# Optimization experiments

Measured on AMD Instinct MI355X. Metric: run time of the kernel, lower is better.

Reference implementation:

```python
import jax, jax.numpy as jnp
import numpy as np

BATCH, SEQ, D_MODEL, D_STATE = 8, 4096, 128, 128


def setup_inputs() -> dict:
    key = jax.random.key(0)
    ks = jax.random.split(key, 6)
    x = jax.random.normal(ks[0], (BATCH, SEQ, D_MODEL), jnp.float32)
    # Stable (negative) eigenvalues so A_discrete = exp(dt*Lambda) < 1 and powers don't overflow.
    Lam = -(jax.random.uniform(ks[1], (D_STATE,), jnp.float32) * 2.0 + 0.1)
    B = jax.random.normal(ks[2], (D_STATE, D_MODEL), jnp.float32) / np.sqrt(D_STATE)
    C = jax.random.normal(ks[3], (D_MODEL, D_STATE), jnp.float32) / np.sqrt(D_STATE)
    Dv = jax.random.normal(ks[4], (D_MODEL,), jnp.float32)
    log_dt = (jax.random.uniform(ks[5], (D_MODEL,), jnp.float32)
              * (np.log(0.001) - np.log(0.1)) + np.log(0.1)).astype(jnp.float32)
    return {"x": x, "Lam": Lam, "B": B, "C": C, "Dv": Dv, "log_dt": log_dt}


def _s4_forward(x, Lam, B, C, Dv, log_dt):
    # x: (batch, L, M) with transposed=False
    _, L, M = x.shape
    dt = jnp.exp(log_dt)                                    # (M,)
    rate = dt[:, None] * Lam[None, :]                       # (M, N) = log(A_discrete)
    ell = jnp.arange(L, dtype=x.dtype)                      # (L,)
    # powers[m, s, l] = A_discrete[m, s] ** l  (closed form of the sequential cumprod)
    powers = jnp.exp(rate[:, :, None] * ell[None, None, :])  # (M, N, L)
    # Original: einsum('ds,msl->dsl', B, powers) sums over m, giving B[d,s]*Psum[s,l];
    # then einsum('md,dsl->ml', C, .) contracts d and s -> kernel = C @ B @ Psum.
    Psum = powers.sum(axis=0)                               # (N, L)
    kernel = C @ (B @ Psum)                                 # (M, L)
    xt = jnp.transpose(x, (0, 2, 1))                        # (B, M, L)
    n = 2 * L  # zero-padded linear convolution via FFT
    y_fft = jnp.fft.rfft(xt, n=n) * jnp.fft.rfft(kernel, n=n)[None]
    y = jnp.fft.irfft(y_fft, n=n)[..., :L]                  # (B, M, L)
    y = y + Dv[None, :, None] * xt                          # skip connection D*u
    return jnp.transpose(y, (0, 2, 1))                      # (B, L, M)


def reference(x, Lam, B, C, Dv, log_dt):
    return _s4_forward(x, Lam, B, C, Dv, log_dt)
```

## Files before the change

### kernel.cpp

```cpp
#include <hip/hip_runtime.h>
#include <math.h>

#define BATCH 8
#define SEQ   4096
#define DM    128
#define DS    128
#define N2    4096
#define NT    256
#define NTP   256

__device__ __forceinline__ float2 cmulf(float2 a, float2 b) {
    return make_float2(a.x * b.x - a.y * b.y, a.x * b.y + a.y * b.x);
}
__device__ __forceinline__ float2 caddf(float2 a, float2 b) { return make_float2(a.x + b.x, a.y + b.y); }
__device__ __forceinline__ float2 csubf(float2 a, float2 b) { return make_float2(a.x - b.x, a.y - b.y); }
__device__ __forceinline__ float2 conjf2(float2 a) { return make_float2(a.x, -a.y); }
__device__ __forceinline__ float2 cisf(float t) { float s, c; __sincosf(t, &s, &c); return make_float2(c, s); }

__device__ __forceinline__ int nibrev(int k) { return ((k & 15) << 8) | (k & 0xF0) | (k >> 8); }
__device__ __forceinline__ int physi(int a) { return a ^ ((a >> 4) & 15); }
__device__ __forceinline__ int pqslot(int p) { return ((p & 15) << 8) | (p >> 4); }

__device__ __forceinline__ void dft16_fwd(const float2 x[16], float2 Xh[16]) {
    const float2 W[10] = { {1.f,0.f},
        {0.92387953f,-0.38268343f},{0.70710678f,-0.70710678f},{0.38268343f,-0.92387953f},
        {0.f,-1.f},{-0.38268343f,-0.92387953f},{-0.70710678f,-0.70710678f},
        {-0.92387953f,-0.38268343f},{-1.f,0.f},{-0.92387953f,0.38268343f} };
    float2 y[16];
#pragma unroll
    for (int j = 0; j < 4; ++j) {
        float2 a0 = x[j], a1 = x[j+4], a2 = x[j+8], a3 = x[j+12];
        float2 t0 = caddf(a0,a2), t1 = csubf(a0,a2);
        float2 t2 = caddf(a1,a3), t3 = csubf(a1,a3);
        float2 b1 = make_float2(t1.x + t3.y, t1.y - t3.x);
        float2 b3 = make_float2(t1.x - t3.y, t1.y + t3.x);
        y[j]    = caddf(t0,t2);
        y[j+4]  = cmulf(b1, W[j]);
        y[j+8]  = cmulf(csubf(t0,t2), W[2*j]);
        y[j+12] = cmulf(b3, W[3*j]);
    }
#pragma unroll
    for (int g = 0; g < 4; ++g) {
        float2 a0 = y[4*g], a1 = y[4*g+1], a2 = y[4*g+2], a3 = y[4*g+3];
        float2 t0 = caddf(a0,a2), t1 = csubf(a0,a2);
        float2 t2 = caddf(a1,a3), t3 = csubf(a1,a3);
        Xh[4*g]   = caddf(t0,t2);
        Xh[4*g+1] = make_float2(t1.x + t3.y, t1.y - t3.x);
        Xh[4*g+2] = csubf(t0,t2);
        Xh[4*g+3] = make_float2(t1.x - t3.y, t1.y + t3.x);
    }
}
__device__ __forceinline__ void dft16_inv(const float2 x[16], float2 Xh[16]) {
    const float2 W[10] = { {1.f,0.f},
        {0.92387953f,0.38268343f},{0.70710678f,0.70710678f},{0.38268343f,0.92387953f},
        {0.f,1.f},{-0.38268343f,0.92387953f},{-0.70710678f,0.70710678f},
        {-0.92387953f,0.38268343f},{-1.f,0.f},{-0.92387953f,-0.38268343f} };
    float2 y[16];
#pragma unroll
    for (int j = 0; j < 4; ++j) {
        float2 a0 = x[j], a1 = x[j+4], a2 = x[j+8], a3 = x[j+12];
        float2 t0 = caddf(a0,a2), t1 = csubf(a0,a2);
        float2 t2 = caddf(a1,a3), t3 = csubf(a1,a3);
        float2 b1 = make_float2(t1.x - t3.y, t1.y + t3.x);
        float2 b3 = make_float2(t1.x + t3.y, t1.y - t3.x);
        y[j]    = caddf(t0,t2);
        y[j+4]  = cmulf(b1, W[j]);
        y[j+8]  = cmulf(csubf(t0,t2), W[2*j]);
        y[j+12] = cmulf(b3, W[3*j]);
    }
#pragma unroll
    for (int g = 0; g < 4; ++g) {
        float2 a0 = y[4*g], a1 = y[4*g+1], a2 = y[4*g+2], a3 = y[4*g+3];
        float2 t0 = caddf(a0,a2), t1 = csubf(a0,a2);
        float2 t2 = caddf(a1,a3), t3 = csubf(a1,a3);
        Xh[4*g]   = caddf(t0,t2);
        Xh[4*g+1] = make_float2(t1.x - t3.y, t1.y + t3.x);
        Xh[4*g+2] = csubf(t0,t2);
        Xh[4*g+3] = make_float2(t1.x + t3.y, t1.y - t3.x);
    }
}


template<int Q>
__device__ __forceinline__ void stage_fwd(float2* z, int t) {
    float2 x[16], Xh[16];
    int adr[16];
    if (Q == 16) {
        int j = t & 15, top = t >> 4;
#pragma unroll
        for (int r = 0; r < 16; ++r) adr[r] = (top << 8) + (r << 4) + (j ^ r);
    } else {
        int j4 = t & 15;
#pragma unroll
        for (int r = 0; r < 16; ++r) adr[r] = (t << 4) + (j4 ^ r);
    }
#pragma unroll
    for (int r = 0; r < 16; ++r) x[r] = z[adr[r]];
    dft16_fwd(x, Xh);
    if (Q > 1) {
        int j = t & (Q - 1);
        float2 w1 = cisf(-(float)M_PI / (8.0f * (float)Q) * (float)j);
        float2 w = make_float2(1.f, 0.f);
#pragma unroll
        for (int k = 0; k < 16; ++k) {
            int sk = ((k & 3) << 2) | (k >> 2);
            z[adr[k]] = cmulf(Xh[sk], w);
            w = cmulf(w, w1);
        }
    } else {
#pragma unroll
        for (int k = 0; k < 16; ++k) {
            int sk = ((k & 3) << 2) | (k >> 2);
            z[adr[k]] = Xh[sk];
        }
    }
}

template<int Q>
__device__ __forceinline__ void stage_inv(float2* z, int t) {
    float2 x[16], Xh[16];
    int adr[16];
    if (Q == 16) {
        int j = t & 15, top = t >> 4;
#pragma unroll
        for (int r = 0; r < 16; ++r) adr[r] = (top << 8) + (r << 4) + (j ^ r);
    } else {
        int j4 = t & 15;
#pragma unroll
        for (int r = 0; r < 16; ++r) adr[r] = (t << 4) + (j4 ^ r);
    }
    if (Q > 1) {
        int j = t & (Q - 1);
        float2 w1 = cisf((float)M_PI / (8.0f * (float)Q) * (float)j);
        float2 w = make_float2(1.f, 0.f);
#pragma unroll
        for (int k = 0; k < 16; ++k) {
            x[k] = cmulf(z[adr[k]], w);
            w = cmulf(w, w1);
        }
    } else {
#pragma unroll
        for (int k = 0; k < 16; ++k) x[k] = z[adr[k]];
    }
    dft16_inv(x, Xh);
#pragma unroll
    for (int r = 0; r < 16; ++r) {
        int sr = ((r & 3) << 2) | (r >> 2);
        z[adr[r]] = Xh[sr];
    }
}

__device__ __forceinline__ void fwd_first(float2* z, const float2* __restrict__ vrow, int t) {
    float2 x[16], Xh[16];
#pragma unroll
    for (int r = 0; r < 8; ++r) x[r] = vrow[t + (r << 8)];
#pragma unroll
    for (int r = 8; r < 16; ++r) x[r] = make_float2(0.f, 0.f);
    dft16_fwd(x, Xh);
    int b0 = t ^ ((t >> 4) & 15);
    float2 w1 = cisf(-(float)M_PI / 2048.0f * (float)t);
    float2 w = make_float2(1.f, 0.f);
#pragma unroll
    for (int k = 0; k < 16; ++k) {
        int sk = ((k & 3) << 2) | (k >> 2);
        z[b0 + (k << 8)] = cmulf(Xh[sk], w);
        w = cmulf(w, w1);
    }
}

__device__ __forceinline__ void inv_last_store(const float2* z, float2* __restrict__ xrow,
                                               int t, float dv) {
    float2 x[16], Xh[16];
    int b0 = t ^ ((t >> 4) & 15);
    float2 w1 = cisf((float)M_PI / 2048.0f * (float)t);
    float2 w = make_float2(1.f, 0.f);
#pragma unroll
    for (int k = 0; k < 16; ++k) {
        x[k] = cmulf(z[b0 + (k << 8)], w);
        w = cmulf(w, w1);
    }
    dft16_inv(x, Xh);
    const float invN = 1.0f / 4096.0f;
#pragma unroll
    for (int r = 0; r < 8; ++r) {
        int sr = ((r & 3) << 2) | (r >> 2);
        float2 res = Xh[sr];
        float2 xv = xrow[t + (r << 8)];
        xrow[t + (r << 8)] = make_float2(res.x * invN + dv * xv.x, res.y * invN + dv * xv.y);
    }
}

__device__ __forceinline__ void pq_one(float2 Kk, float2 Kkp, float thk,
                                       float2 fap, float2 fbp,
                                       float2* P, float2* Q) {
    float2 e  = cisf(-thk);
    float2 fa = make_float2(0.5f * (1.f + e.y), -0.5f * e.x);
    float2 fb = make_float2(0.5f * (1.f - e.y),  0.5f * e.x);
    float2 ak = cmulf(Kk, fa), bk = cmulf(Kk, fb);
    float2 apv = cmulf(Kkp, fap), bpv = cmulf(Kkp, fbp);
    float2 g = make_float2(0.5f * (1.f + e.y), 0.5f * e.x);
    float2 h = make_float2(0.5f * (1.f - e.y), -0.5f * e.x);
    *P = caddf(cmulf(g, ak), cmulf(h, conjf2(bpv)));
    *Q = caddf(cmulf(g, bk), cmulf(h, conjf2(apv)));
}
__device__ __forceinline__ void pq_pair(float2 Kk, float2 Kkp, float thk, float thkp,
                                        float2* Pk, float2* Qk, float2* Pkp, float2* Qkp) {
    float2 e  = cisf(-thk);
    float2 ep = cisf(-thkp);
    float2 fa  = make_float2(0.5f * (1.f + e.y),  -0.5f * e.x);
    float2 fb  = make_float2(0.5f * (1.f - e.y),   0.5f * e.x);
    float2 fap = make_float2(0.5f * (1.f + ep.y), -0.5f * ep.x);
    float2 fbp = make_float2(0.5f * (1.f - ep.y),  0.5f * ep.x);
    pq_one(Kk,  Kkp, thk,  fap, fbp, Pk,  Qk);
    pq_one(Kkp, Kk,  thkp, fa,  fb,  Pkp, Qkp);
}

__global__ void __launch_bounds__(NTP) prep_GP(
    const float* __restrict__ Lam, const float* __restrict__ logdt, float* __restrict__ Psum,
    const float* __restrict__ Cm, const float* __restrict__ Bm, float* __restrict__ GT) {
    int bid = blockIdx.x, t = threadIdx.x;
    if (bid < 256) {
        __shared__ float E[DM];
        int s = bid >> 1, half = bid & 1;
        if (t < DM) E[t] = __expf(logdt[t]) * Lam[s];
        __syncthreads();
        int l0 = t + 2048 * half;
        float acc[8] = {0.f,0.f,0.f,0.f,0.f,0.f,0.f,0.f};
        for (int m = 0; m < DM; ++m) {
            float e = E[m];
            float w = __expf(e * (float)l0);
            float r = __expf(e * 256.0f);
#pragma unroll
            for (int i = 0; i < 8; ++i) { acc[i] += w; w *= r; }
        }
#pragma unroll
        for (int i = 0; i < 8; ++i) Psum[s * SEQ + l0 + 256 * i] = acc[i];
    } else {
        int gid = (bid - 256) * NTP + t;
        int m = gid >> 7, j = gid & 127;
        float acc = 0.f;
        for (int i = 0; i < DS; ++i) acc += Cm[m * DS + i] * Bm[i * DM + j];
        GT[j * DM + m] = acc;
    }
}

__global__ void prep_K2(const float* __restrict__ GT, const float* __restrict__ Psum,
                        float* __restrict__ K) {
    __shared__ float4 PT[DS][4];
    int l0 = blockIdx.x * 16;
    int t = threadIdx.x;
    for (int idx = t; idx < 512; idx += NTP) {
        int s = idx >> 2, q = idx & 3;
        PT[s][q] = ((const float4*)(Psum + s * SEQ + l0))[q];
    }
    __syncthreads();
    int m = t & 127, half = t >> 7;
    float acc[8] = {0.f,0.f,0.f,0.f,0.f,0.f,0.f,0.f};
    for (int s = 0; s < DS; ++s) {
        float g = GT[s * DM + m];
        float4 p0 = PT[s][half * 2], p1 = PT[s][half * 2 + 1];
        acc[0] += g * p0.x; acc[1] += g * p0.y; acc[2] += g * p0.z; acc[3] += g * p0.w;
        acc[4] += g * p1.x; acc[5] += g * p1.y; acc[6] += g * p1.z; acc[7] += g * p1.w;
    }
    float4* kp = (float4*)(K + (size_t)m * SEQ + l0 + half * 8);
    kp[0] = make_float4(acc[0], acc[1], acc[2], acc[3]);
    kp[1] = make_float4(acc[4], acc[5], acc[6], acc[7]);
}

__global__ void __launch_bounds__(NT, 4) fftK_PQ(const float* __restrict__ K,
                                                 float4* __restrict__ PQ) {
    __shared__ __align__(16) float2 z[N2];
    int t = threadIdx.x, m = blockIdx.x;
    const float2* krow = (const float2*)(K + (size_t)m * SEQ);

    fwd_first(z, krow, t);  __syncthreads();
    stage_fwd<16>(z, t);    __syncthreads();
    stage_fwd<1>(z, t);     __syncthreads();

    float4* dst = PQ + (size_t)m * 4096;
#pragma unroll
    for (int c = 0; c < 8; ++c) {
        int pos = (t << 4) | c;
        float2 Pk, Qk, Pkp, Qkp;
        if (pos == 0) {
            float2 v0 = z[0];
            float2 v2 = z[8];
            float2 Ku0    = make_float2(v0.x + v0.y, 0.f);
            float2 Ku4096 = make_float2(v0.x - v0.y, 0.f);
            float2 Ku2048 = conjf2(v2);
            float2 Pd, Qd;
            pq_pair(Ku0, Ku4096, 0.f, (float)M_PI, &Pk, &Qk, &Pd, &Qd);
            float th2 = 0.5f * (float)M_PI;
            pq_pair(Ku2048, Ku2048, th2, th2, &Pkp, &Qkp, &Pd, &Qd);
            dst[pqslot(0)] = make_float4(Pk.x, Pk.y, Qk.x, Qk.y);
            dst[pqslot(8)] = make_float4(Pkp.x, Pkp.y, Qkp.x, Qkp.y);
        } else {
            int k  = nibrev(pos);
            int kp = 4096 - k;
            int ppos = nibrev(kp);
            float2 va = z[physi(pos)];
            float2 vb = z[physi(ppos)];
            float thk  = (float)M_PI * (float)k / 4096.0f;
            float thkp = (float)M_PI - thk;
            float2 e  = cisf(-thk);
            float2 cb = conjf2(vb);
            float2 s  = caddf(va, cb), d = csubf(va, cb);
            float2 pr = cmulf(e, d);
            float2 Kuk = make_float2(0.5f * (s.x + pr.y), 0.5f * (s.y - pr.x));
            float2 ep = make_float2(-e.x, e.y);
            float2 ca = conjf2(va);
            float2 s2 = caddf(vb, ca), d2 = csubf(vb, ca);
            float2 p2 = cmulf(ep, d2);
            float2 Kukp = make_float2(0.5f * (s2.x + p2.y), 0.5f * (s2.y - p2.x));
            pq_pair(Kuk, Kukp, thk, thkp, &Pk, &Qk, &Pkp, &Qkp);
            dst[pqslot(pos)]  = make_float4(Pk.x, Pk.y, Qk.x, Qk.y);
            dst[pqslot(ppos)] = make_float4(Pkp.x, Pkp.y, Qkp.x, Qkp.y);
        }
    }
}

__global__ void __launch_bounds__(NT, 4) conv16(float* __restrict__ xt,
                                                const float4* __restrict__ PQ,
                                                const float* __restrict__ Dv) {
    __shared__ __align__(16) float2 z[N2];
    int t = threadIdx.x;
    int m = blockIdx.x & (DM - 1);
    int b = blockIdx.x >> 7;
    float2* xrow = (float2*)(xt + (((size_t)b * DM + m) << 12));

    fwd_first(z, xrow, t);  __syncthreads();
    stage_fwd<16>(z, t);    __syncthreads();
    stage_fwd<1>(z, t);     __syncthreads();

    float2 x[16];
    {
        const float4* pq = PQ + (size_t)m * 4096;
        int j4 = t & 15;
#pragma unroll
        for (int r = 0; r < 16; ++r) {
            int pos = (t << 4) | r;
            float2 va = z[(t << 4) + (r ^ j4)];
            int k  = nibrev(pos);
            int kp = (4096 - k) & 4095;
            float2 vb = z[physi(nibrev(kp))];
            float4 co = pq[(r << 8) | t];
            x[r] = caddf(cmulf(make_float2(co.x, co.y), va),
                         cmulf(make_float2(co.z, co.w), conjf2(vb)));
        }
    }
    __syncthreads();
    {
        float2 Xh[16];
        dft16_inv(x, Xh);
        int j4 = t & 15;
#pragma unroll
        for (int r = 0; r < 16; ++r) {
            int sr = ((r & 3) << 2) | (r >> 2);
            z[(t << 4) + (r ^ j4)] = Xh[sr];
        }
    }
    __syncthreads();

    stage_inv<16>(z, t);    __syncthreads();
    inv_last_store(z, xrow, t, Dv[m]);
}

__global__ void transpose_xin(const float* __restrict__ x, float* __restrict__ xt) {
    __shared__ float tile[32][33];
    int b = blockIdx.z;
    int l0 = blockIdx.x * 32, m0 = blockIdx.y * 32;
    int t = threadIdx.x;
    int lr = t >> 3, mc4 = (t & 7) * 4;
    float4 v = *(const float4*)&x[(size_t)b * SEQ * DM + (size_t)(l0 + lr) * DM + m0 + mc4];
    tile[lr][mc4 + 0] = v.x; tile[lr][mc4 + 1] = v.y;
    tile[lr][mc4 + 2] = v.z; tile[lr][mc4 + 3] = v.w;
    __syncthreads();
    int mr = t >> 3, lc4 = (t & 7) * 4;
    float4 o = make_float4(tile[lc4 + 0][mr], tile[lc4 + 1][mr],
                           tile[lc4 + 2][mr], tile[lc4 + 3][mr]);
    *(float4*)&xt[(size_t)b * DM * SEQ + (size_t)(m0 + mr) * SEQ + l0 + lc4] = o;
}

__global__ void transpose_yout(const float* __restrict__ yt, float* __restrict__ out) {
    __shared__ float tile[32][33];
    int b = blockIdx.z;
    int l0 = blockIdx.x * 32, m0 = blockIdx.y * 32;
    int t = threadIdx.x;
    int mr = t >> 3, lc4 = (t & 7) * 4;
    float4 v = *(const float4*)&yt[(size_t)b * DM * SEQ + (size_t)(m0 + mr) * SEQ + l0 + lc4];
    tile[mr][lc4 + 0] = v.x; tile[mr][lc4 + 1] = v.y;
    tile[mr][lc4 + 2] = v.z; tile[mr][lc4 + 3] = v.w;
    __syncthreads();
    int lr = t >> 3, mc4 = (t & 7) * 4;
    float4 o = make_float4(tile[mc4 + 0][lr], tile[mc4 + 1][lr],
                           tile[mc4 + 2][lr], tile[mc4 + 3][lr]);
    *(float4*)&out[(size_t)b * SEQ * DM + (size_t)(l0 + lr) * DM + m0 + mc4] = o;
}

extern "C" void kernel_launch(void* const* d_in, const int* in_sizes, int n_in,
                              void* d_out, int out_size, void* d_ws, size_t ws_size,
                              hipStream_t stream) {
    const float* x     = (const float*)d_in[0];
    const float* Lam   = (const float*)d_in[1];
    const float* Bm    = (const float*)d_in[2];
    const float* Cm    = (const float*)d_in[3];
    const float* Dv    = (const float*)d_in[4];
    const float* logdt = (const float*)d_in[5];
    float* out = (float*)d_out;

    float*  ws   = (float*)d_ws;
    float*  xt   = ws;
    float4* PQ   = (float4*)(ws + 4194304);
    float*  K    = ws + 4194304 + 2097152;
    float*  Psum = K + 524288;
    float*  GT   = Psum + 524288;

    hipLaunchKernelGGL(prep_GP,        dim3(320),        dim3(NTP),  0, stream,
                       Lam, logdt, Psum, Cm, Bm, GT);
    hipLaunchKernelGGL(prep_K2,        dim3(256),        dim3(NTP),  0, stream, GT, Psum, K);
    hipLaunchKernelGGL(fftK_PQ,        dim3(128),        dim3(NT),   0, stream, K, PQ);
    hipLaunchKernelGGL(transpose_xin,  dim3(128, 4, 8),  dim3(NT),   0, stream, x, xt);
    hipLaunchKernelGGL(conv16,         dim3(1024),       dim3(NT),   0, stream, xt, PQ, Dv);
    hipLaunchKernelGGL(transpose_yout, dim3(128, 4, 8),  dim3(NT),   0, stream, xt, out);
}
```

Before: 129.8 us.

## Fuse input transpose into prep kernel and prune FFT butterflies

Merges the input transpose into the prep kernel launch, which removes one kernel launch. It specializes the radix-16 stages: the forward first stage skips the zero-padded half and the inverse last stage computes only the eight outputs that are kept. The first-stage output stays in registers so it is not reloaded from shared memory, and twiddles come from two half-length recurrences. fftK_PQ is split across twice as many blocks, each handling half of the PQ epilogue; the forward FFT of K is now computed redundantly in both blocks.

```diff
diff --git a/kernel.cpp b/kernel.cpp
--- a/kernel.cpp
+++ b/kernel.cpp
@@ -21,6 +21,31 @@
 __device__ __forceinline__ int physi(int a) { return a ^ ((a >> 4) & 15); }
 __device__ __forceinline__ int pqslot(int p) { return ((p & 15) << 8) | (p >> 4); }
 
+__device__ __forceinline__ void dft16_fwd_l2(const float2 y[16], float2 Xh[16]) {
+#pragma unroll
+    for (int g = 0; g < 4; ++g) {
+        float2 a0 = y[4*g], a1 = y[4*g+1], a2 = y[4*g+2], a3 = y[4*g+3];
+        float2 t0 = caddf(a0,a2), t1 = csubf(a0,a2);
+        float2 t2 = caddf(a1,a3), t3 = csubf(a1,a3);
+        Xh[4*g]   = caddf(t0,t2);
+        Xh[4*g+1] = make_float2(t1.x + t3.y, t1.y - t3.x);
+        Xh[4*g+2] = csubf(t0,t2);
+        Xh[4*g+3] = make_float2(t1.x - t3.y, t1.y + t3.x);
+    }
+}
+__device__ __forceinline__ void dft16_inv_l2(const float2 y[16], float2 Xh[16]) {
+#pragma unroll
+    for (int g = 0; g < 4; ++g) {
+        float2 a0 = y[4*g], a1 = y[4*g+1], a2 = y[4*g+2], a3 = y[4*g+3];
+        float2 t0 = caddf(a0,a2), t1 = csubf(a0,a2);
+        float2 t2 = caddf(a1,a3), t3 = csubf(a1,a3);
+        Xh[4*g]   = caddf(t0,t2);
+        Xh[4*g+1] = make_float2(t1.x - t3.y, t1.y + t3.x);
+        Xh[4*g+2] = csubf(t0,t2);
+        Xh[4*g+3] = make_float2(t1.x + t3.y, t1.y - t3.x);
+    }
+}
+
 __device__ __forceinline__ void dft16_fwd(const float2 x[16], float2 Xh[16]) {
     const float2 W[10] = { {1.f,0.f},
         {0.92387953f,-0.38268343f},{0.70710678f,-0.70710678f},{0.38268343f,-0.92387953f},
@@ -39,17 +64,28 @@
         y[j+8]  = cmulf(csubf(t0,t2), W[2*j]);
         y[j+12] = cmulf(b3, W[3*j]);
     }
-#pragma unroll
-    for (int g = 0; g < 4; ++g) {
-        float2 a0 = y[4*g], a1 = y[4*g+1], a2 = y[4*g+2], a3 = y[4*g+3];
-        float2 t0 = caddf(a0,a2), t1 = csubf(a0,a2);
-        float2 t2 = caddf(a1,a3), t3 = csubf(a1,a3);
-        Xh[4*g]   = caddf(t0,t2);
-        Xh[4*g+1] = make_float2(t1.x + t3.y, t1.y - t3.x);
-        Xh[4*g+2] = csubf(t0,t2);
-        Xh[4*g+3] = make_float2(t1.x - t3.y, t1.y + t3.x);
-    }
-}
+    dft16_fwd_l2(y, Xh);
+}
+
+__device__ __forceinline__ void dft16_fwd_zh(const float2 x[8], float2 Xh[16]) {
+    const float2 W[10] = { {1.f,0.f},
+        {0.92387953f,-0.38268343f},{0.70710678f,-0.70710678f},{0.38268343f,-0.92387953f},
+        {0.f,-1.f},{-0.38268343f,-0.92387953f},{-0.70710678f,-0.70710678f},
+        {-0.92387953f,-0.38268343f},{-1.f,0.f},{-0.92387953f,0.38268343f} };
+    float2 y[16];
+#pragma unroll
+    for (int j = 0; j < 4; ++j) {
+        float2 a0 = x[j], a1 = x[j+4];
+        float2 b1 = make_float2(a0.x + a1.y, a0.y - a1.x);
+        float2 b3 = make_float2(a0.x - a1.y, a0.y + a1.x);
+        y[j]    = caddf(a0, a1);
+        y[j+4]  = cmulf(b1, W[j]);
+        y[j+8]  = cmulf(csubf(a0, a1), W[2*j]);
+        y[j+12] = cmulf(b3, W[3*j]);
+    }
+    dft16_fwd_l2(y, Xh);
+}
+
 __device__ __forceinline__ void dft16_inv(const float2 x[16], float2 Xh[16]) {
     const float2 W[10] = { {1.f,0.f},
         {0.92387953f,0.38268343f},{0.70710678f,0.70710678f},{0.38268343f,0.92387953f},
@@ -68,79 +104,76 @@
         y[j+8]  = cmulf(csubf(t0,t2), W[2*j]);
         y[j+12] = cmulf(b3, W[3*j]);
     }
+    dft16_inv_l2(y, Xh);
+}
+
+__device__ __forceinline__ void dft16_inv_lo8(const float2 x[16], float2 out8[8]) {
+    const float2 W[10] = { {1.f,0.f},
+        {0.92387953f,0.38268343f},{0.70710678f,0.70710678f},{0.38268343f,0.92387953f},
+        {0.f,1.f},{-0.38268343f,0.92387953f},{-0.70710678f,0.70710678f},
+        {-0.92387953f,0.38268343f},{-1.f,0.f},{-0.92387953f,-0.38268343f} };
+    float2 y[16];
+#pragma unroll
+    for (int j = 0; j < 4; ++j) {
+        float2 a0 = x[j], a1 = x[j+4], a2 = x[j+8], a3 = x[j+12];
+        float2 t0 = caddf(a0,a2), t1 = csubf(a0,a2);
+        float2 t2 = caddf(a1,a3), t3 = csubf(a1,a3);
+        float2 b1 = make_float2(t1.x - t3.y, t1.y + t3.x);
+        float2 b3 = make_float2(t1.x + t3.y, t1.y - t3.x);
+        y[j]    = caddf(t0,t2);
+        y[j+4]  = cmulf(b1, W[j]);
+        y[j+8]  = cmulf(csubf(t0,t2), W[2*j]);
+        y[j+12] = cmulf(b3, W[3*j]);
+    }
 #pragma unroll
     for (int g = 0; g < 4; ++g) {
         float2 a0 = y[4*g], a1 = y[4*g+1], a2 = y[4*g+2], a3 = y[4*g+3];
         float2 t0 = caddf(a0,a2), t1 = csubf(a0,a2);
         float2 t2 = caddf(a1,a3), t3 = csubf(a1,a3);
-        Xh[4*g]   = caddf(t0,t2);
-        Xh[4*g+1] = make_float2(t1.x - t3.y, t1.y + t3.x);
-        Xh[4*g+2] = csubf(t0,t2);
-        Xh[4*g+3] = make_float2(t1.x + t3.y, t1.y - t3.x);
-    }
-}
-
-
-template<int Q>
-__device__ __forceinline__ void stage_fwd(float2* z, int t) {
+        out8[g]   = caddf(t0,t2);
+        out8[4+g] = make_float2(t1.x - t3.y, t1.y + t3.x);
+    }
+}
+
+__device__ __forceinline__ void stage16_fwd(float2* z, int t) {
     float2 x[16], Xh[16];
     int adr[16];
-    if (Q == 16) {
-        int j = t & 15, top = t >> 4;
-#pragma unroll
-        for (int r = 0; r < 16; ++r) adr[r] = (top << 8) + (r << 4) + (j ^ r);
-    } else {
-        int j4 = t & 15;
-#pragma unroll
-        for (int r = 0; r < 16; ++r) adr[r] = (t << 4) + (j4 ^ r);
-    }
+    int j = t & 15, top = t >> 4;
+#pragma unroll
+    for (int r = 0; r < 16; ++r) adr[r] = (top << 8) + (r << 4) + (j ^ r);
 #pragma unroll
     for (int r = 0; r < 16; ++r) x[r] = z[adr[r]];
     dft16_fwd(x, Xh);
-    if (Q > 1) {
-        int j = t & (Q - 1);
-        float2 w1 = cisf(-(float)M_PI / (8.0f * (float)Q) * (float)j);
-        float2 w = make_float2(1.f, 0.f);
-#pragma unroll
-        for (int k = 0; k < 16; ++k) {
-            int sk = ((k & 3) << 2) | (k >> 2);
-            z[adr[k]] = cmulf(Xh[sk], w);
-            w = cmulf(w, w1);
-        }
-    } else {
-#pragma unroll
-        for (int k = 0; k < 16; ++k) {
-            int sk = ((k & 3) << 2) | (k >> 2);
-            z[adr[k]] = Xh[sk];
-        }
-    }
-}
-
-template<int Q>
-__device__ __forceinline__ void stage_inv(float2* z, int t) {
+    float ang = -(float)M_PI / 128.0f * (float)j;
+    float2 w1 = cisf(ang);
+    float2 wa = make_float2(1.f, 0.f);
+    float2 wb = cisf(ang * 8.0f);
+#pragma unroll
+    for (int k = 0; k < 8; ++k) {
+        int sk = ((k & 3) << 2) | (k >> 2);
+        z[adr[k]]     = cmulf(Xh[sk],     wa);
+        z[adr[k + 8]] = cmulf(Xh[sk + 2], wb);
+        wa = cmulf(wa, w1);
+        wb = cmulf(wb, w1);
+    }
+}
+
+__device__ __forceinline__ void stage16_inv(float2* z, int t) {
     float2 x[16], Xh[16];
     int adr[16];
-    if (Q == 16) {
-        int j = t & 15, top = t >> 4;
-#pragma unroll
-        for (int r = 0; r < 16; ++r) adr[r] = (top << 8) + (r << 4) + (j ^ r);
-    } else {
-        int j4 = t & 15;
-#pragma unroll
-        for (int r = 0; r < 16; ++r) adr[r] = (t << 4) + (j4 ^ r);
-    }
-    if (Q > 1) {
-        int j = t & (Q - 1);
-        float2 w1 = cisf((float)M_PI / (8.0f * (float)Q) * (float)j);
-        float2 w = make_float2(1.f, 0.f);
-#pragma unroll
-        for (int k = 0; k < 16; ++k) {
-            x[k] = cmulf(z[adr[k]], w);
-            w = cmulf(w, w1);
-        }
-    } else {
-#pragma unroll
-        for (int k = 0; k < 16; ++k) x[k] = z[adr[k]];
+    int j = t & 15, top = t >> 4;
+#pragma unroll
+    for (int r = 0; r < 16; ++r) adr[r] = (top << 8) + (r << 4) + (j ^ r);
+    float ang = (float)M_PI / 128.0f * (float)j;
+    float2 w1 = cisf(ang);
+    float2 wa = make_float2(1.f, 0.f);
+    float2 wb = cisf(ang * 8.0f);
+#pragma unroll
+    for (int k = 0; k < 8; ++k) {
+        x[k]     = cmulf(z[adr[k]],     wa);
+        x[k + 8] = cmulf(z[adr[k + 8]], wb);
+        wa = cmulf(wa, w1);
+        wb = cmulf(wb, w1);
     }
     dft16_inv(x, Xh);
 #pragma unroll
@@ -150,50 +183,71 @@
     }
 }
 
-__device__ __forceinline__ void fwd_first(float2* z, const float2* __restrict__ vrow, int t) {
+__device__ __forceinline__ void stage1_fwd_keep(float2* z, int t, float2 v[16]) {
     float2 x[16], Xh[16];
-#pragma unroll
-    for (int r = 0; r < 8; ++r) x[r] = vrow[t + (r << 8)];
-#pragma unroll
-    for (int r = 8; r < 16; ++r) x[r] = make_float2(0.f, 0.f);
+    int adr[16];
+    int j4 = t & 15;
+#pragma unroll
+    for (int r = 0; r < 16; ++r) adr[r] = (t << 4) + (j4 ^ r);
+#pragma unroll
+    for (int r = 0; r < 16; ++r) x[r] = z[adr[r]];
     dft16_fwd(x, Xh);
-    int b0 = t ^ ((t >> 4) & 15);
-    float2 w1 = cisf(-(float)M_PI / 2048.0f * (float)t);
-    float2 w = make_float2(1.f, 0.f);
 #pragma unroll
     for (int k = 0; k < 16; ++k) {
         int sk = ((k & 3) << 2) | (k >> 2);
-        z[b0 + (k << 8)] = cmulf(Xh[sk], w);
-        w = cmulf(w, w1);
+        v[k] = Xh[sk];
+        z[adr[k]] = v[k];
+    }
+}
+
+__device__ __forceinline__ void fwd_first(float2* z, const float2* __restrict__ vrow, int t) {
+    float2 x8[8], Xh[16];
+#pragma unroll
+    for (int r = 0; r < 8; ++r) x8[r] = vrow[t + (r << 8)];
+    dft16_fwd_zh(x8, Xh);
+    int b0 = t ^ ((t >> 4) & 15);
+    float ang = -(float)M_PI / 2048.0f * (float)t;
+    float2 w1 = cisf(ang);
+    float2 wa = make_float2(1.f, 0.f);
+    float2 wb = cisf(ang * 8.0f);
+#pragma unroll
+    for (int k = 0; k < 8; ++k) {
+        int sk = ((k & 3) << 2) | (k >> 2);
+        z[b0 + (k << 8)]       = cmulf(Xh[sk],     wa);
+        z[b0 + ((k + 8) << 8)] = cmulf(Xh[sk + 2], wb);
+        wa = cmulf(wa, w1);
+        wb = cmulf(wb, w1);
     }
 }
 
 __device__ __forceinline__ void inv_last_store(const float2* z, float2* __restrict__ xrow,
                                                int t, float dv) {
-    float2 x[16], Xh[16];
+    float2 x[16], out8[8];
     int b0 = t ^ ((t >> 4) & 15);
-    float2 w1 = cisf((float)M_PI / 2048.0f * (float)t);
-    float2 w = make_float2(1.f, 0.f);
-#pragma unroll
-    for (int k = 0; k < 16; ++k) {
-        x[k] = cmulf(z[b0 + (k << 8)], w);
-        w = cmulf(w, w1);
-    }
-    dft16_inv(x, Xh);
+    float ang = (float)M_PI / 2048.0f * (float)t;
+    float2 w1 = cisf(ang);
+    float2 wa = make_float2(1.f, 0.f);
+    float2 wb = cisf(ang * 8.0f);
+#pragma unroll
+    for (int k = 0; k < 8; ++k) {
+        x[k]     = cmulf(z[b0 + (k << 8)],       wa);
+        x[k + 8] = cmulf(z[b0 + ((k + 8) << 8)], wb);
+        wa = cmulf(wa, w1);
+        wb = cmulf(wb, w1);
+    }
+    dft16_inv_lo8(x, out8);
     const float invN = 1.0f / 4096.0f;
 #pragma unroll
     for (int r = 0; r < 8; ++r) {
-        int sr = ((r & 3) << 2) | (r >> 2);
-        float2 res = Xh[sr];
+        float2 res = out8[r];
         float2 xv = xrow[t + (r << 8)];
         xrow[t + (r << 8)] = make_float2(res.x * invN + dv * xv.x, res.y * invN + dv * xv.y);
     }
 }
 
-__device__ __forceinline__ void pq_one(float2 Kk, float2 Kkp, float thk,
-                                       float2 fap, float2 fbp,
-                                       float2* P, float2* Q) {
-    float2 e  = cisf(-thk);
+__device__ __forceinline__ void pq_one_e(float2 Kk, float2 Kkp, float2 e,
+                                         float2 fap, float2 fbp,
+                                         float2* P, float2* Q) {
     float2 fa = make_float2(0.5f * (1.f + e.y), -0.5f * e.x);
     float2 fb = make_float2(0.5f * (1.f - e.y),  0.5f * e.x);
     float2 ak = cmulf(Kk, fa), bk = cmulf(Kk, fb);
@@ -203,24 +257,25 @@
     *P = caddf(cmulf(g, ak), cmulf(h, conjf2(bpv)));
     *Q = caddf(cmulf(g, bk), cmulf(h, conjf2(apv)));
 }
-__device__ __forceinline__ void pq_pair(float2 Kk, float2 Kkp, float thk, float thkp,
-                                        float2* Pk, float2* Qk, float2* Pkp, float2* Qkp) {
-    float2 e  = cisf(-thk);
-    float2 ep = cisf(-thkp);
+__device__ __forceinline__ void pq_pair_e(float2 Kk, float2 Kkp, float2 e,
+                                          float2* Pk, float2* Qk, float2* Pkp, float2* Qkp) {
+    float2 ep = make_float2(-e.x, e.y);
     float2 fa  = make_float2(0.5f * (1.f + e.y),  -0.5f * e.x);
     float2 fb  = make_float2(0.5f * (1.f - e.y),   0.5f * e.x);
     float2 fap = make_float2(0.5f * (1.f + ep.y), -0.5f * ep.x);
     float2 fbp = make_float2(0.5f * (1.f - ep.y),  0.5f * ep.x);
-    pq_one(Kk,  Kkp, thk,  fap, fbp, Pk,  Qk);
-    pq_one(Kkp, Kk,  thkp, fa,  fb,  Pkp, Qkp);
-}
-
-__global__ void __launch_bounds__(NTP) prep_GP(
+    pq_one_e(Kk,  Kkp, e,  fap, fbp, Pk,  Qk);
+    pq_one_e(Kkp, Kk,  ep, fa,  fb,  Pkp, Qkp);
+}
+
+__global__ void __launch_bounds__(NTP) prep_fused(
     const float* __restrict__ Lam, const float* __restrict__ logdt, float* __restrict__ Psum,
-    const float* __restrict__ Cm, const float* __restrict__ Bm, float* __restrict__ GT) {
+    const float* __restrict__ Cm, const float* __restrict__ Bm, float* __restrict__ GT,
+    const float* __restrict__ x, float* __restrict__ xt) {
+    __shared__ float E[DM];
+    __shared__ float tile[32][33];
     int bid = blockIdx.x, t = threadIdx.x;
     if (bid < 256) {
-        __shared__ float E[DM];
         int s = bid >> 1, half = bid & 1;
         if (t < DM) E[t] = __expf(logdt[t]) * Lam[s];
         __syncthreads();
@@ -235,12 +290,26 @@
         }
 #pragma unroll
         for (int i = 0; i < 8; ++i) Psum[s * SEQ + l0 + 256 * i] = acc[i];
-    } else {
+    } else if (bid < 320) {
         int gid = (bid - 256) * NTP + t;
         int m = gid >> 7, j = gid & 127;
         float acc = 0.f;
         for (int i = 0; i < DS; ++i) acc += Cm[m * DS + i] * Bm[i * DM + j];
         GT[j * DM + m] = acc;
+    } else {
+        int u = bid - 320;
+        int b = u >> 9;
+        int m0 = ((u >> 7) & 3) * 32;
+        int l0 = (u & 127) * 32;
+        int lr = t >> 3, mc4 = (t & 7) * 4;
+        float4 v = *(const float4*)&x[(size_t)b * SEQ * DM + (size_t)(l0 + lr) * DM + m0 + mc4];
+        tile[lr][mc4 + 0] = v.x; tile[lr][mc4 + 1] = v.y;
+        tile[lr][mc4 + 2] = v.z; tile[lr][mc4 + 3] = v.w;
+        __syncthreads();
+        int mr = t >> 3, lc4 = (t & 7) * 4;
+        float4 o = make_float4(tile[lc4 + 0][mr], tile[lc4 + 1][mr],
+                               tile[lc4 + 2][mr], tile[lc4 + 3][mr]);
+        *(float4*)&xt[(size_t)b * DM * SEQ + (size_t)(m0 + mr) * SEQ + l0 + lc4] = o;
     }
 }
 
@@ -267,41 +336,33 @@
     kp[1] = make_float4(acc[4], acc[5], acc[6], acc[7]);
 }
 
-__global__ void __launch_bounds__(NT, 4) fftK_PQ(const float* __restrict__ K,
-                                                 float4* __restrict__ PQ) {
-    __shared__ __align__(16) float2 z[N2];
-    int t = threadIdx.x, m = blockIdx.x;
-    const float2* krow = (const float2*)(K + (size_t)m * SEQ);
-
-    fwd_first(z, krow, t);  __syncthreads();
-    stage_fwd<16>(z, t);    __syncthreads();
-    stage_fwd<1>(z, t);     __syncthreads();
-
-    float4* dst = PQ + (size_t)m * 4096;
-#pragma unroll
-    for (int c = 0; c < 8; ++c) {
+template<int C0>
+__device__ __forceinline__ void pq_epilogue(const float2 v[16], const float2* z,
+                                            float4* __restrict__ dst, int t) {
+#pragma unroll
+    for (int cc = 0; cc < 4; ++cc) {
+        const int c = C0 + cc;
         int pos = (t << 4) | c;
         float2 Pk, Qk, Pkp, Qkp;
         if (pos == 0) {
-            float2 v0 = z[0];
-            float2 v2 = z[8];
+            float2 v0 = v[0];
+            float2 v2 = v[8];
             float2 Ku0    = make_float2(v0.x + v0.y, 0.f);
             float2 Ku4096 = make_float2(v0.x - v0.y, 0.f);
             float2 Ku2048 = conjf2(v2);
             float2 Pd, Qd;
-            pq_pair(Ku0, Ku4096, 0.f, (float)M_PI, &Pk, &Qk, &Pd, &Qd);
-            float th2 = 0.5f * (float)M_PI;
-            pq_pair(Ku2048, Ku2048, th2, th2, &Pkp, &Qkp, &Pd, &Qd);
+            pq_pair_e(Ku0, Ku4096, make_float2(1.f, 0.f), &Pk, &Qk, &Pd, &Qd);
+            float2 Pd2, Qd2;
+            pq_pair_e(Ku2048, Ku2048, make_float2(0.f, -1.f), &Pkp, &Qkp, &Pd2, &Qd2);
             dst[pqslot(0)] = make_float4(Pk.x, Pk.y, Qk.x, Qk.y);
             dst[pqslot(8)] = make_float4(Pkp.x, Pkp.y, Qkp.x, Qkp.y);
         } else {
             int k  = nibrev(pos);
             int kp = 4096 - k;
             int ppos = nibrev(kp);
-            float2 va = z[physi(pos)];
+            float2 va = v[c];
             float2 vb = z[physi(ppos)];
-            float thk  = (float)M_PI * (float)k / 4096.0f;
-            float thkp = (float)M_PI - thk;
+            float thk = (float)M_PI * (float)k / 4096.0f;
             float2 e  = cisf(-thk);
             float2 cb = conjf2(vb);
             float2 s  = caddf(va, cb), d = csubf(va, cb);
@@ -312,11 +373,29 @@
             float2 s2 = caddf(vb, ca), d2 = csubf(vb, ca);
             float2 p2 = cmulf(ep, d2);
             float2 Kukp = make_float2(0.5f * (s2.x + p2.y), 0.5f * (s2.y - p2.x));
-            pq_pair(Kuk, Kukp, thk, thkp, &Pk, &Qk, &Pkp, &Qkp);
+            pq_pair_e(Kuk, Kukp, e, &Pk, &Qk, &Pkp, &Qkp);
             dst[pqslot(pos)]  = make_float4(Pk.x, Pk.y, Qk.x, Qk.y);
             dst[pqslot(ppos)] = make_float4(Pkp.x, Pkp.y, Qkp.x, Qkp.y);
         }
     }
+}
+
+__global__ void __launch_bounds__(NT, 4) fftK_PQ(const float* __restrict__ K,
+                                                 float4* __restrict__ PQ) {
+    __shared__ __align__(16) float2 z[N2];
+    int t = threadIdx.x;
+    int m = blockIdx.x & (DM - 1);
+    int half = blockIdx.x >> 7;
+    const float2* krow = (const float2*)(K + (size_t)m * SEQ);
+
+    fwd_first(z, krow, t);  __syncthreads();
+    stage16_fwd(z, t);      __syncthreads();
+    float2 v[16];
+    stage1_fwd_keep(z, t, v); __syncthreads();
+
+    float4* dst = PQ + (size_t)m * 4096;
+    if (half == 0) pq_epilogue<0>(v, z, dst, t);
+    else           pq_epilogue<4>(v, z, dst, t);
 }
 
 __global__ void __launch_bounds__(NT, 4) conv16(float* __restrict__ xt,
@@ -329,29 +408,27 @@
     float2* xrow = (float2*)(xt + (((size_t)b * DM + m) << 12));
 
     fwd_first(z, xrow, t);  __syncthreads();
-    stage_fwd<16>(z, t);    __syncthreads();
-    stage_fwd<1>(z, t);     __syncthreads();
-
-    float2 x[16];
+    stage16_fwd(z, t);      __syncthreads();
+    float2 v[16];
+    stage1_fwd_keep(z, t, v); __syncthreads();
+
     {
         const float4* pq = PQ + (size_t)m * 4096;
-        int j4 = t & 15;
 #pragma unroll
         for (int r = 0; r < 16; ++r) {
             int pos = (t << 4) | r;
-            float2 va = z[(t << 4) + (r ^ j4)];
             int k  = nibrev(pos);
             int kp = (4096 - k) & 4095;
             float2 vb = z[physi(nibrev(kp))];
             float4 co = pq[(r << 8) | t];
-            x[r] = caddf(cmulf(make_float2(co.x, co.y), va),
+            v[r] = caddf(cmulf(make_float2(co.x, co.y), v[r]),
                          cmulf(make_float2(co.z, co.w), conjf2(vb)));
         }
     }
     __syncthreads();
     {
         float2 Xh[16];
-        dft16_inv(x, Xh);
+        dft16_inv(v, Xh);
         int j4 = t & 15;
 #pragma unroll
         for (int r = 0; r < 16; ++r) {
@@ -361,24 +438,8 @@
     }
     __syncthreads();
 
-    stage_inv<16>(z, t);    __syncthreads();
+    stage16_inv(z, t);      __syncthreads();
     inv_last_store(z, xrow, t, Dv[m]);
-}
-
-__global__ void transpose_xin(const float* __restrict__ x, float* __restrict__ xt) {
-    __shared__ float tile[32][33];
-    int b = blockIdx.z;
-    int l0 = blockIdx.x * 32, m0 = blockIdx.y * 32;
-    int t = threadIdx.x;
-    int lr = t >> 3, mc4 = (t & 7) * 4;
-    float4 v = *(const float4*)&x[(size_t)b * SEQ * DM + (size_t)(l0 + lr) * DM + m0 + mc4];
-    tile[lr][mc4 + 0] = v.x; tile[lr][mc4 + 1] = v.y;
-    tile[lr][mc4 + 2] = v.z; tile[lr][mc4 + 3] = v.w;
-    __syncthreads();
-    int mr = t >> 3, lc4 = (t & 7) * 4;
-    float4 o = make_float4(tile[lc4 + 0][mr], tile[lc4 + 1][mr],
-                           tile[lc4 + 2][mr], tile[lc4 + 3][mr]);
-    *(float4*)&xt[(size_t)b * DM * SEQ + (size_t)(m0 + mr) * SEQ + l0 + lc4] = o;
 }
 
 __global__ void transpose_yout(const float* __restrict__ yt, float* __restrict__ out) {
@@ -415,11 +476,10 @@
     float*  Psum = K + 524288;
     float*  GT   = Psum + 524288;
 
-    hipLaunchKernelGGL(prep_GP,        dim3(320),        dim3(NTP),  0, stream,
-                       Lam, logdt, Psum, Cm, Bm, GT);
+    hipLaunchKernelGGL(prep_fused,     dim3(4416),       dim3(NTP),  0, stream,
+                       Lam, logdt, Psum, Cm, Bm, GT, x, xt);
     hipLaunchKernelGGL(prep_K2,        dim3(256),        dim3(NTP),  0, stream, GT, Psum, K);
-    hipLaunchKernelGGL(fftK_PQ,        dim3(128),        dim3(NT),   0, stream, K, PQ);
-    hipLaunchKernelGGL(transpose_xin,  dim3(128, 4, 8),  dim3(NT),   0, stream, x, xt);
+    hipLaunchKernelGGL(fftK_PQ,        dim3(256),        dim3(NT),   0, stream, K, PQ);
     hipLaunchKernelGGL(conv16,         dim3(1024),       dim3(NT),   0, stream, xt, PQ, Dv);
     hipLaunchKernelGGL(transpose_yout, dim3(128, 4, 8),  dim3(NT),   0, stream, xt, out);
 }
```

Result: faster. 124.5 us (-4.1%).
